# Performance work log

Measured on AMD Instinct MI355X. Metric: run time of the kernel, lower is better.

## Reference

```python
import jax, jax.numpy as jnp
import numpy as np


def setup_inputs() -> dict:
    key = jax.random.key(0)
    k1, k2 = jax.random.split(key)
    B, C, H, W = 16, 256, 64, 64
    K, D = 1024, 256
    z = jax.random.normal(k1, (B, C, H, W), dtype=jnp.float32)
    embedding = jax.random.normal(k2, (K, D), dtype=jnp.float32)
    return {"z": z, "embedding": embedding}


def reference(z, embedding):
    # _preprocess: shift channel dim (axis 1) to last, flatten -> [N, D]
    B, C, H, W = z.shape
    encoded_permuted = jnp.transpose(z, (0, 2, 3, 1))  # [B, H, W, C]
    permuted_shape = encoded_permuted.shape
    encoded_flat = encoded_permuted.reshape(-1, C)  # [N, D]

    x_sq = jnp.sum(encoded_flat * encoded_flat, axis=1, keepdims=True)  # [N, 1]
    e_sq = jnp.sum(embedding * embedding, axis=1)  # [K]
    cross = encoded_flat @ embedding.T  # [N, K]
    distances = x_sq - 2.0 * cross + e_sq[None, :]
    codebook_indices = jnp.argmin(distances, axis=1)  # [N]
    quantized_lookup = embedding[codebook_indices]  # [N, D]

    # straight-through estimator
    quantized_flat = encoded_flat + jax.lax.stop_gradient(quantized_lookup - encoded_flat)

    # _postprocess: reshape and shift last dim back to axis 1
    quantized = jnp.transpose(quantized_flat.reshape(permuted_shape), (0, 3, 1, 2))
    return (encoded_flat, quantized_flat, codebook_indices, quantized)
```

## Files before the change

kernel.cpp:

```cpp
#include <hip/hip_runtime.h>
#include <hip/hip_bf16.h>

typedef _Float16 h8 __attribute__((ext_vector_type(8)));
typedef float f4 __attribute__((ext_vector_type(4)));

#define N_TOK 65536
#define DIM 256
#define KCODES 1024
#define HWSZ 4096

__device__ __forceinline__ void gll16(const void* g, void* l) {
    __builtin_amdgcn_global_load_lds((const __attribute__((address_space(1))) void*)g,
                                     (__attribute__((address_space(3))) void*)l, 16, 0, 0);
}


__global__ void k_prep_frag(const float* __restrict__ emb, _Float16* __restrict__ BhF,
                            _Float16* __restrict__ BlF) {
    int gi = blockIdx.x * 256 + threadIdx.x;
    int kb = gi >> 9, s = (gi >> 6) & 7, dq = (gi >> 4) & 3, r = gi & 15;
    int code = kb * 16 + r;
    const float* src = emb + (size_t)code * DIM + s * 32 + dq * 8;
    float4 x0 = *(const float4*)(src);
    float4 x1 = *(const float4*)(src + 4);
    float xs[8] = {x0.x, x0.y, x0.z, x0.w, x1.x, x1.y, x1.z, x1.w};
    h8 hi, lo;
#pragma unroll
    for (int j = 0; j < 8; ++j) {
        _Float16 h = (_Float16)xs[j];
        hi[j] = h;
        lo[j] = (_Float16)(xs[j] - (float)h);
    }
    *(h8*)(BhF + (size_t)gi * 8) = hi;
    *(h8*)(BlF + (size_t)gi * 8) = lo;
}

__global__ void k_esq(const float* __restrict__ emb, float* __restrict__ e_sq) {
    int t = threadIdx.x;
    int code = blockIdx.x * 4 + (t >> 6);
    int l = t & 63;
    float4 v = *(const float4*)(emb + (size_t)code * DIM + l * 4);
    float s = v.x * v.x + v.y * v.y + v.z * v.z + v.w * v.w;
#pragma unroll
    for (int off = 32; off >= 1; off >>= 1) s += __shfl_xor(s, off);
    if (l == 0) e_sq[code] = s;
}

__global__ void k_transpose(const float* __restrict__ z, float* __restrict__ enc,
                            _Float16* __restrict__ AhF, _Float16* __restrict__ AlF) {
    __shared__ float T[64][65];
    int blk = blockIdx.x;
    int b = blk >> 8;
    int rem = blk & 255;
    int c0 = (rem >> 6) * 64;
    int hw0 = (rem & 63) * 64;
    int t = threadIdx.x;
    const float* zp = z + (size_t)b * DIM * HWSZ;
    {
        int hw4 = (t & 15) * 4, cl = t >> 4;
#pragma unroll
        for (int i = 0; i < 4; ++i) {
            int c = cl + i * 16;
            float4 v = *(const float4*)(zp + (size_t)(c0 + c) * HWSZ + hw0 + hw4);
            T[c][hw4 + 0] = v.x; T[c][hw4 + 1] = v.y;
            T[c][hw4 + 2] = v.z; T[c][hw4 + 3] = v.w;
        }
    }
    __syncthreads();
    {
        int c4 = (t & 15) * 4, hwl = t >> 4;
#pragma unroll
        for (int i = 0; i < 4; ++i) {
            int hw = hwl + i * 16;
            float4 v;
            v.x = T[c4 + 0][hw]; v.y = T[c4 + 1][hw];
            v.z = T[c4 + 2][hw]; v.w = T[c4 + 3][hw];
            *(float4*)(enc + (size_t)(b * HWSZ + hw0 + hw) * DIM + c0 + c4) = v;
        }
    }
    {
        int base_nb = b * 256 + (hw0 >> 4);
#pragma unroll
        for (int i = 0; i < 2; ++i) {
            int gidx = i * 256 + t;
            int nbi = gidx >> 7, si = (gidx >> 6) & 1, dq = (gidx >> 4) & 3, r = gidx & 15;
            int hwl = nbi * 16 + r;
            int cl = si * 32 + dq * 8;
            h8 hi, lo;
#pragma unroll
            for (int j = 0; j < 8; ++j) {
                float x = T[cl + j][hwl];
                _Float16 h = (_Float16)x;
                hi[j] = h;
                lo[j] = (_Float16)(x - (float)h);
            }
            size_t G = (((size_t)(base_nb + nbi) * 8) + (c0 >> 5) + si) * 64 + dq * 16 + r;
            *(h8*)(AhF + G * 8) = hi;
            *(h8*)(AlF + G * 8) = lo;
        }
    }
}

#define WAITV(n) asm volatile("s_waitcnt vmcnt(" #n ")" ::: "memory")
#define BARRIER __builtin_amdgcn_s_barrier()
#define PRIO1 __builtin_amdgcn_s_setprio(1)
#define PRIO0 __builtin_amdgcn_s_setprio(0)

extern __shared__ char SB[];

__global__ __launch_bounds__(1024)
void k_gemm_argmin(const _Float16* __restrict__ AhF, const _Float16* __restrict__ AlF,
                   const _Float16* __restrict__ BhF, const _Float16* __restrict__ BlF,
                   const float* __restrict__ e_sq,
                   float* __restrict__ pV1, int* __restrict__ pI1) {
    int gid = blockIdx.x;
    int grp = gid >> 7;
    int colTile = (gid >> 5) & 3;
    int rowTile = grp * 32 + (gid & 31);
    int r0 = rowTile * 256, c0 = colTile * 256;
    int t = threadIdx.x;
    int w = t >> 6, l = t & 63;
    int wm = w >> 2, wn = w & 3;
    int l16 = l & 15, lhi = l >> 4;

    const char* gAh = (const char*)AhF + (((size_t)(rowTile * 16 + w)) << 13) + (l << 4);
    const char* gAl = (const char*)AlF + (((size_t)(rowTile * 16 + w)) << 13) + (l << 4);
    const char* gBh = (const char*)BhF + (((size_t)(colTile * 16 + w)) << 13) + (l << 4);
    const char* gBl = (const char*)BlF + (((size_t)(colTile * 16 + w)) << 13) + (l << 4);

#define ISSUE_S(s) do { \
    char* bp_ = SB + ((s) & 1) * 65536; \
    gll16(gAh + ((s) << 10), bp_ + (w << 10)); \
    gll16(gBh + ((s) << 10), bp_ + 16384 + (w << 10)); \
    gll16(gAl + ((s) << 10), bp_ + 32768 + (w << 10)); \
    gll16(gBl + ((s) << 10), bp_ + 49152 + (w << 10)); \
} while (0)

#define MFMA16(A_, B_) { _Pragma("unroll") for (int mf = 0; mf < 4; ++mf) \
    _Pragma("unroll") for (int nf = 0; nf < 4; ++nf) \
        acc[mf][nf] = __builtin_amdgcn_mfma_f32_16x16x32_f16(A_[mf], B_[nf], acc[mf][nf], 0, 0, 0); }

#define PHASE(q, DO_ISSUE) { \
    WAITV(0); \
    BARRIER; \
    if (DO_ISSUE) ISSUE_S((q) + 1); \
    const char* bp_ = SB + ((q) & 1) * 65536; \
    _Pragma("unroll") for (int mf = 0; mf < 4; ++mf) \
        ah[mf] = *(const h8*)(bp_ + ((wm * 4 + mf) << 10) + (l << 4)); \
    _Pragma("unroll") for (int nf = 0; nf < 4; ++nf) \
        bh[nf] = *(const h8*)(bp_ + 16384 + ((wn * 4 + nf) << 10) + (l << 4)); \
    PRIO1; MFMA16(ah, bh); PRIO0; \
    { h8 xl[4]; \
      _Pragma("unroll") for (int nf = 0; nf < 4; ++nf) \
          xl[nf] = *(const h8*)(bp_ + 49152 + ((wn * 4 + nf) << 10) + (l << 4)); \
      PRIO1; MFMA16(ah, xl); PRIO0; \
      _Pragma("unroll") for (int mf = 0; mf < 4; ++mf) \
          xl[mf] = *(const h8*)(bp_ + 32768 + ((wm * 4 + mf) << 10) + (l << 4)); \
      PRIO1; MFMA16(xl, bh); PRIO0; } }

    f4 acc[4][4];
#pragma unroll
    for (int i = 0; i < 4; ++i)
#pragma unroll
        for (int j = 0; j < 4; ++j) acc[i][j] = (f4)0.0f;

    h8 ah[4], bh[4];

    ISSUE_S(0);

    PHASE(0, 1)  PHASE(1, 1)  PHASE(2, 1)  PHASE(3, 1)
    PHASE(4, 1)  PHASE(5, 1)  PHASE(6, 1)  PHASE(7, 0)

    float* smV = (float*)SB;
    int* smI = (int*)(SB + 4096);

    float esq[4];
#pragma unroll
    for (int nf = 0; nf < 4; ++nf) esq[nf] = e_sq[c0 + wn * 64 + nf * 16 + l16];

#pragma unroll
    for (int mf = 0; mf < 4; ++mf) {
#pragma unroll
        for (int rg = 0; rg < 4; ++rg) {
            float bestV = 3.4e38f;
            int bestI = 0;
#pragma unroll
            for (int nf = 0; nf < 4; ++nf) {
                float v = esq[nf] - 2.0f * acc[mf][nf][rg];
                int ci = c0 + wn * 64 + nf * 16 + l16;
                if (v < bestV || (v == bestV && ci < bestI)) { bestV = v; bestI = ci; }
            }
#pragma unroll
            for (int off = 1; off < 16; off <<= 1) {
                float vv = __shfl_xor(bestV, off);
                int ii = __shfl_xor(bestI, off);
                if (vv < bestV || (vv == bestV && ii < bestI)) { bestV = vv; bestI = ii; }
            }
            if (l16 == 0) {
                int rloc = wm * 64 + mf * 16 + lhi * 4 + rg;
                smV[wn * 256 + rloc] = bestV;
                smI[wn * 256 + rloc] = bestI;
            }
        }
    }
    __syncthreads();
    if (t < 256) {
        float bestV = smV[t];
        int bestI = smI[t];
#pragma unroll
        for (int wn2 = 1; wn2 < 4; ++wn2) {
            float v = smV[wn2 * 256 + t];
            int i2 = smI[wn2 * 256 + t];
            if (v < bestV || (v == bestV && i2 < bestI)) { bestV = v; bestI = i2; }
        }
        pV1[colTile * N_TOK + r0 + t] = bestV;
        pI1[colTile * N_TOK + r0 + t] = bestI;
    }
}

__global__ void k_final_all(const float* __restrict__ pV1, const int* __restrict__ pI1,
                            const float* __restrict__ emb,
                            float* __restrict__ out2, float* __restrict__ out1,
                            float* __restrict__ out3) {
    __shared__ int sidx[256];
    __shared__ float E[32][257];
    int t = threadIdx.x;
    int n0 = blockIdx.x * 256;
    int n = n0 + t;
    float v1 = pV1[n];
    int i1 = pI1[n];
#pragma unroll
    for (int ct = 1; ct < 4; ++ct) {
        float a1 = pV1[ct * N_TOK + n];
        int ai = pI1[ct * N_TOK + n];
        if (a1 < v1 || (a1 == v1 && ai < i1)) { v1 = a1; i1 = ai; }
    }
    out2[n] = (float)i1;
    sidx[t] = i1;
    __syncthreads();
    {
        int rr = t >> 2, q = t & 3;
#pragma unroll
        for (int i = 0; i < 4; ++i) {
            int r = i * 64 + rr;
            int idx = sidx[r];
            const float* src = emb + (size_t)idx * DIM + q * 64;
            float* dst = out1 + (size_t)(n0 + r) * DIM + q * 64;
#pragma unroll
            for (int j = 0; j < 16; ++j)
                *(float4*)(dst + j * 4) = *(const float4*)(src + j * 4);
        }
    }
    int b = n0 >> 12;
    int hw0b = n0 & 4095;
    for (int sub = 0; sub < 8; ++sub) {
        __syncthreads();
        {
            int r = t >> 3, oct = t & 7;
            int idx = sidx[sub * 32 + r];
            const float* src = emb + (size_t)idx * DIM + oct * 32;
#pragma unroll
            for (int i = 0; i < 8; ++i) {
                float4 v = *(const float4*)(src + i * 4);
                E[r][oct * 32 + i * 4 + 0] = v.x;
                E[r][oct * 32 + i * 4 + 1] = v.y;
                E[r][oct * 32 + i * 4 + 2] = v.z;
                E[r][oct * 32 + i * 4 + 3] = v.w;
            }
        }
        __syncthreads();
        {
            int w = t >> 6, l = t & 63;
            int ch = l >> 5, hw = l & 31;
            float* dst = out3 + (size_t)b * DIM * HWSZ + hw0b + sub * 32 + hw;
#pragma unroll
            for (int it = 0; it < 32; ++it) {
                int c = w * 64 + it * 2 + ch;
                dst[(size_t)c * HWSZ] = E[hw][c];
            }
        }
    }
}

extern "C" void kernel_launch(void* const* d_in, const int* in_sizes, int n_in,
                              void* d_out, int out_size, void* d_ws, size_t ws_size,
                              hipStream_t stream) {
    const float* z = (const float*)d_in[0];
    const float* emb = (const float*)d_in[1];
    float* out = (float*)d_out;
    float* out0 = out;
    float* out1 = out + 16777216;
    float* out2 = out + 33554432;
    float* out3 = out + 33619968;

    _Float16* AhF = (_Float16*)out1;
    _Float16* AlF = (_Float16*)(out1 + 8388608);

    char* ws = (char*)d_ws;
    _Float16* BhF = (_Float16*)(ws);
    _Float16* BlF = (_Float16*)(ws + 524288);
    float* e_sq = (float*)(ws + 1048576);
    float* pV1 = (float*)(ws + 1052672);
    int* pI1 = (int*)(ws + 2101248);

    hipFuncSetAttribute((const void*)k_gemm_argmin,
                        hipFuncAttributeMaxDynamicSharedMemorySize, 131072);

    k_prep_frag<<<128, 256, 0, stream>>>(emb, BhF, BlF);
    k_esq<<<256, 256, 0, stream>>>(emb, e_sq);
    k_transpose<<<4096, 256, 0, stream>>>(z, out0, AhF, AlF);
    k_gemm_argmin<<<1024, 1024, 131072, stream>>>(AhF, AlF, BhF, BlF, e_sq, pV1, pI1);
    k_final_all<<<256, 256, 0, stream>>>(pV1, pI1, emb, out2, out1, out3);
}
```

Measured before the change: 205.4 us.

## Shrink GEMM tiles to 128x128 and merge argmin partials via packed 64-bit atomicMin

The fused distance-GEMM/argmin kernel moves from 256x256 tiles with 1024 threads to 128x128 tiles with 512 threads and 64KB LDS, so more blocks can be resident per CU. Per-tile minima are packed into an order-preserving 64-bit key (float bits, then index) and merged with atomicMin into one array. The key array is initialised inside the e_sq kernel. This replaces the four-way partial arrays and simplifies the final gather kernel, which now handles 64 tokens per block. In exchange, the smaller tiles reload A and B more often per unit of compute, and the change adds atomic traffic.

```diff
diff --git a/kernel.cpp b/kernel.cpp
--- a/kernel.cpp
+++ b/kernel.cpp
@@ -35,8 +35,10 @@
     *(h8*)(BlF + (size_t)gi * 8) = lo;
 }
 
-__global__ void k_esq(const float* __restrict__ emb, float* __restrict__ e_sq) {
+__global__ void k_esq(const float* __restrict__ emb, float* __restrict__ e_sq,
+                      unsigned long long* __restrict__ key64) {
     int t = threadIdx.x;
+    key64[blockIdx.x * 256 + t] = ~0ull;
     int code = blockIdx.x * 4 + (t >> 6);
     int l = t & 63;
     float4 v = *(const float4*)(emb + (size_t)code * DIM + l * 4);
@@ -108,63 +110,64 @@
 
 extern __shared__ char SB[];
 
-__global__ __launch_bounds__(1024)
+__global__ __launch_bounds__(512, 4)
 void k_gemm_argmin(const _Float16* __restrict__ AhF, const _Float16* __restrict__ AlF,
                    const _Float16* __restrict__ BhF, const _Float16* __restrict__ BlF,
                    const float* __restrict__ e_sq,
-                   float* __restrict__ pV1, int* __restrict__ pI1) {
+                   unsigned long long* __restrict__ key64) {
     int gid = blockIdx.x;
-    int grp = gid >> 7;
-    int colTile = (gid >> 5) & 3;
-    int rowTile = grp * 32 + (gid & 31);
-    int r0 = rowTile * 256, c0 = colTile * 256;
+    int grp = gid >> 9;
+    int colTile = (gid >> 6) & 7;
+    int rowTile = grp * 64 + (gid & 63);
+    int r0 = rowTile * 128, c0 = colTile * 128;
     int t = threadIdx.x;
     int w = t >> 6, l = t & 63;
     int wm = w >> 2, wn = w & 3;
     int l16 = l & 15, lhi = l >> 4;
 
-    const char* gAh = (const char*)AhF + (((size_t)(rowTile * 16 + w)) << 13) + (l << 4);
-    const char* gAl = (const char*)AlF + (((size_t)(rowTile * 16 + w)) << 13) + (l << 4);
-    const char* gBh = (const char*)BhF + (((size_t)(colTile * 16 + w)) << 13) + (l << 4);
-    const char* gBl = (const char*)BlF + (((size_t)(colTile * 16 + w)) << 13) + (l << 4);
+    const char* gAh = (const char*)AhF + (((size_t)(rowTile * 8 + w)) << 13) + (l << 4);
+    const char* gAl = (const char*)AlF + (((size_t)(rowTile * 8 + w)) << 13) + (l << 4);
+    const char* gBh = (const char*)BhF + (((size_t)(colTile * 8 + w)) << 13) + (l << 4);
+    const char* gBl = (const char*)BlF + (((size_t)(colTile * 8 + w)) << 13) + (l << 4);
 
 #define ISSUE_S(s) do { \
-    char* bp_ = SB + ((s) & 1) * 65536; \
+    char* bp_ = SB + ((s) & 1) * 32768; \
     gll16(gAh + ((s) << 10), bp_ + (w << 10)); \
-    gll16(gBh + ((s) << 10), bp_ + 16384 + (w << 10)); \
-    gll16(gAl + ((s) << 10), bp_ + 32768 + (w << 10)); \
-    gll16(gBl + ((s) << 10), bp_ + 49152 + (w << 10)); \
+    gll16(gBh + ((s) << 10), bp_ + 8192 + (w << 10)); \
+    gll16(gAl + ((s) << 10), bp_ + 16384 + (w << 10)); \
+    gll16(gBl + ((s) << 10), bp_ + 24576 + (w << 10)); \
 } while (0)
 
-#define MFMA16(A_, B_) { _Pragma("unroll") for (int mf = 0; mf < 4; ++mf) \
-    _Pragma("unroll") for (int nf = 0; nf < 4; ++nf) \
+#define MFMA8(A_, B_) { _Pragma("unroll") for (int mf = 0; mf < 4; ++mf) \
+    _Pragma("unroll") for (int nf = 0; nf < 2; ++nf) \
         acc[mf][nf] = __builtin_amdgcn_mfma_f32_16x16x32_f16(A_[mf], B_[nf], acc[mf][nf], 0, 0, 0); }
 
 #define PHASE(q, DO_ISSUE) { \
     WAITV(0); \
     BARRIER; \
     if (DO_ISSUE) ISSUE_S((q) + 1); \
-    const char* bp_ = SB + ((q) & 1) * 65536; \
+    const char* bp_ = SB + ((q) & 1) * 32768; \
     _Pragma("unroll") for (int mf = 0; mf < 4; ++mf) \
         ah[mf] = *(const h8*)(bp_ + ((wm * 4 + mf) << 10) + (l << 4)); \
-    _Pragma("unroll") for (int nf = 0; nf < 4; ++nf) \
-        bh[nf] = *(const h8*)(bp_ + 16384 + ((wn * 4 + nf) << 10) + (l << 4)); \
-    PRIO1; MFMA16(ah, bh); PRIO0; \
-    { h8 xl[4]; \
-      _Pragma("unroll") for (int nf = 0; nf < 4; ++nf) \
-          xl[nf] = *(const h8*)(bp_ + 49152 + ((wn * 4 + nf) << 10) + (l << 4)); \
-      PRIO1; MFMA16(ah, xl); PRIO0; \
+    _Pragma("unroll") for (int nf = 0; nf < 2; ++nf) \
+        bh[nf] = *(const h8*)(bp_ + 8192 + ((wn * 2 + nf) << 10) + (l << 4)); \
+    PRIO1; MFMA8(ah, bh); PRIO0; \
+    { h8 xb[2]; \
+      _Pragma("unroll") for (int nf = 0; nf < 2; ++nf) \
+          xb[nf] = *(const h8*)(bp_ + 24576 + ((wn * 2 + nf) << 10) + (l << 4)); \
+      PRIO1; MFMA8(ah, xb); PRIO0; } \
+    { h8 xa[4]; \
       _Pragma("unroll") for (int mf = 0; mf < 4; ++mf) \
-          xl[mf] = *(const h8*)(bp_ + 32768 + ((wm * 4 + mf) << 10) + (l << 4)); \
-      PRIO1; MFMA16(xl, bh); PRIO0; } }
-
-    f4 acc[4][4];
+          xa[mf] = *(const h8*)(bp_ + 16384 + ((wm * 4 + mf) << 10) + (l << 4)); \
+      PRIO1; MFMA8(xa, bh); PRIO0; } }
+
+    f4 acc[4][2];
 #pragma unroll
     for (int i = 0; i < 4; ++i)
 #pragma unroll
-        for (int j = 0; j < 4; ++j) acc[i][j] = (f4)0.0f;
-
-    h8 ah[4], bh[4];
+        for (int j = 0; j < 2; ++j) acc[i][j] = (f4)0.0f;
+
+    h8 ah[4], bh[2];
 
     ISSUE_S(0);
 
@@ -172,11 +175,11 @@
     PHASE(4, 1)  PHASE(5, 1)  PHASE(6, 1)  PHASE(7, 0)
 
     float* smV = (float*)SB;
-    int* smI = (int*)(SB + 4096);
-
-    float esq[4];
-#pragma unroll
-    for (int nf = 0; nf < 4; ++nf) esq[nf] = e_sq[c0 + wn * 64 + nf * 16 + l16];
+    int* smI = (int*)(SB + 2048);
+
+    float esq[2];
+#pragma unroll
+    for (int nf = 0; nf < 2; ++nf) esq[nf] = e_sq[c0 + wn * 32 + nf * 16 + l16];
 
 #pragma unroll
     for (int mf = 0; mf < 4; ++mf) {
@@ -185,9 +188,9 @@
             float bestV = 3.4e38f;
             int bestI = 0;
 #pragma unroll
-            for (int nf = 0; nf < 4; ++nf) {
+            for (int nf = 0; nf < 2; ++nf) {
                 float v = esq[nf] - 2.0f * acc[mf][nf][rg];
-                int ci = c0 + wn * 64 + nf * 16 + l16;
+                int ci = c0 + wn * 32 + nf * 16 + l16;
                 if (v < bestV || (v == bestV && ci < bestI)) { bestV = v; bestI = ci; }
             }
 #pragma unroll
@@ -198,62 +201,54 @@
             }
             if (l16 == 0) {
                 int rloc = wm * 64 + mf * 16 + lhi * 4 + rg;
-                smV[wn * 256 + rloc] = bestV;
-                smI[wn * 256 + rloc] = bestI;
+                smV[wn * 128 + rloc] = bestV;
+                smI[wn * 128 + rloc] = bestI;
             }
         }
     }
     __syncthreads();
-    if (t < 256) {
+    if (t < 128) {
         float bestV = smV[t];
         int bestI = smI[t];
 #pragma unroll
         for (int wn2 = 1; wn2 < 4; ++wn2) {
-            float v = smV[wn2 * 256 + t];
-            int i2 = smI[wn2 * 256 + t];
+            float v = smV[wn2 * 128 + t];
+            int i2 = smI[wn2 * 128 + t];
             if (v < bestV || (v == bestV && i2 < bestI)) { bestV = v; bestI = i2; }
         }
-        pV1[colTile * N_TOK + r0 + t] = bestV;
-        pI1[colTile * N_TOK + r0 + t] = bestI;
-    }
-}
-
-__global__ void k_final_all(const float* __restrict__ pV1, const int* __restrict__ pI1,
+        unsigned int bu = __float_as_uint(bestV);
+        unsigned int u = (bu & 0x80000000u) ? ~bu : (bu | 0x80000000u);
+        unsigned long long key = ((unsigned long long)u << 10) | (unsigned int)bestI;
+        atomicMin(&key64[r0 + t], key);
+    }
+}
+
+__global__ void k_final_all(const unsigned long long* __restrict__ key64,
                             const float* __restrict__ emb,
                             float* __restrict__ out2, float* __restrict__ out1,
                             float* __restrict__ out3) {
-    __shared__ int sidx[256];
+    __shared__ int sidx[64];
     __shared__ float E[32][257];
     int t = threadIdx.x;
-    int n0 = blockIdx.x * 256;
-    int n = n0 + t;
-    float v1 = pV1[n];
-    int i1 = pI1[n];
-#pragma unroll
-    for (int ct = 1; ct < 4; ++ct) {
-        float a1 = pV1[ct * N_TOK + n];
-        int ai = pI1[ct * N_TOK + n];
-        if (a1 < v1 || (a1 == v1 && ai < i1)) { v1 = a1; i1 = ai; }
-    }
-    out2[n] = (float)i1;
-    sidx[t] = i1;
+    int n0 = blockIdx.x * 64;
+    if (t < 64) {
+        int idx = (int)(key64[n0 + t] & 1023ull);
+        out2[n0 + t] = (float)idx;
+        sidx[t] = idx;
+    }
     __syncthreads();
     {
-        int rr = t >> 2, q = t & 3;
-#pragma unroll
-        for (int i = 0; i < 4; ++i) {
-            int r = i * 64 + rr;
-            int idx = sidx[r];
-            const float* src = emb + (size_t)idx * DIM + q * 64;
-            float* dst = out1 + (size_t)(n0 + r) * DIM + q * 64;
-#pragma unroll
-            for (int j = 0; j < 16; ++j)
-                *(float4*)(dst + j * 4) = *(const float4*)(src + j * 4);
-        }
+        int r = t >> 2, q = t & 3;
+        int idx = sidx[r];
+        const float* src = emb + (size_t)idx * DIM + q * 64;
+        float* dst = out1 + (size_t)(n0 + r) * DIM + q * 64;
+#pragma unroll
+        for (int j = 0; j < 16; ++j)
+            *(float4*)(dst + j * 4) = *(const float4*)(src + j * 4);
     }
     int b = n0 >> 12;
     int hw0b = n0 & 4095;
-    for (int sub = 0; sub < 8; ++sub) {
+    for (int sub = 0; sub < 2; ++sub) {
         __syncthreads();
         {
             int r = t >> 3, oct = t & 7;
@@ -300,15 +295,14 @@
     _Float16* BhF = (_Float16*)(ws);
     _Float16* BlF = (_Float16*)(ws + 524288);
     float* e_sq = (float*)(ws + 1048576);
-    float* pV1 = (float*)(ws + 1052672);
-    int* pI1 = (int*)(ws + 2101248);
+    unsigned long long* key64 = (unsigned long long*)(ws + 1052672);
 
     hipFuncSetAttribute((const void*)k_gemm_argmin,
-                        hipFuncAttributeMaxDynamicSharedMemorySize, 131072);
+                        hipFuncAttributeMaxDynamicSharedMemorySize, 65536);
 
     k_prep_frag<<<128, 256, 0, stream>>>(emb, BhF, BlF);
-    k_esq<<<256, 256, 0, stream>>>(emb, e_sq);
+    k_esq<<<256, 256, 0, stream>>>(emb, e_sq, key64);
     k_transpose<<<4096, 256, 0, stream>>>(z, out0, AhF, AlF);
-    k_gemm_argmin<<<1024, 1024, 131072, stream>>>(AhF, AlF, BhF, BlF, e_sq, pV1, pI1);
-    k_final_all<<<256, 256, 0, stream>>>(pV1, pI1, emb, out2, out1, out3);
-}
+    k_gemm_argmin<<<4096, 512, 65536, stream>>>(AhF, AlF, BhF, BlF, e_sq, key64);
+    k_final_all<<<1024, 256, 0, stream>>>(key64, emb, out2, out1, out3);
+}
```

Result: slower. 253.2 us (+23.3%).

## Restructure GEMM-argmin into 8-wave blocks with 4-stage split-precision pipeline

Applied to the files above, without the earlier changes.

The fused distance GEMM now runs 512 threads per block instead of 1024, with each wave computing 128x64 outputs (8x4 MFMA tiles) instead of 64x64. The three split-fp16 products (hi*hi, hi*lo, lo*hi) are flattened into 24 K-chunks, each fed by a 4-deep LDS ring buffer. A and B prefetches are issued separately in the two halves of each chunk. The goal is more register-level reuse of B fragments and deeper overlap of global-to-LDS loads with MFMA work. The cost is doubled accumulator registers per wave and more barriers per chunk. The launch_bounds(512,2) hint cannot be met with 128KB of LDS per block.

```diff
diff --git a/kernel.cpp b/kernel.cpp
--- a/kernel.cpp
+++ b/kernel.cpp
@@ -105,10 +105,12 @@
 #define BARRIER __builtin_amdgcn_s_barrier()
 #define PRIO1 __builtin_amdgcn_s_setprio(1)
 #define PRIO0 __builtin_amdgcn_s_setprio(0)
+#define LGKM0 asm volatile("s_waitcnt lgkmcnt(0)" ::: "memory")
+#define SGB0 __builtin_amdgcn_sched_barrier(0)
 
 extern __shared__ char SB[];
 
-__global__ __launch_bounds__(1024)
+__global__ __launch_bounds__(512, 2)
 void k_gemm_argmin(const _Float16* __restrict__ AhF, const _Float16* __restrict__ AlF,
                    const _Float16* __restrict__ BhF, const _Float16* __restrict__ BlF,
                    const float* __restrict__ e_sq,
@@ -123,53 +125,59 @@
     int wm = w >> 2, wn = w & 3;
     int l16 = l & 15, lhi = l >> 4;
 
-    const char* gAh = (const char*)AhF + (((size_t)(rowTile * 16 + w)) << 13) + (l << 4);
-    const char* gAl = (const char*)AlF + (((size_t)(rowTile * 16 + w)) << 13) + (l << 4);
-    const char* gBh = (const char*)BhF + (((size_t)(colTile * 16 + w)) << 13) + (l << 4);
-    const char* gBl = (const char*)BlF + (((size_t)(colTile * 16 + w)) << 13) + (l << 4);
-
-#define ISSUE_S(s) do { \
-    char* bp_ = SB + ((s) & 1) * 65536; \
-    gll16(gAh + ((s) << 10), bp_ + (w << 10)); \
-    gll16(gBh + ((s) << 10), bp_ + 16384 + (w << 10)); \
-    gll16(gAl + ((s) << 10), bp_ + 32768 + (w << 10)); \
-    gll16(gBl + ((s) << 10), bp_ + 49152 + (w << 10)); \
-} while (0)
-
-#define MFMA16(A_, B_) { _Pragma("unroll") for (int mf = 0; mf < 4; ++mf) \
+    const char* gAh = (const char*)AhF + (((size_t)(rowTile * 16 + 2 * w)) << 13) + (l << 4);
+    const char* gAl = (const char*)AlF + (((size_t)(rowTile * 16 + 2 * w)) << 13) + (l << 4);
+    const char* gBh = (const char*)BhF + (((size_t)(colTile * 16 + 2 * w)) << 13) + (l << 4);
+    const char* gBl = (const char*)BlF + (((size_t)(colTile * 16 + 2 * w)) << 13) + (l << 4);
+
+#define ISSUE_A(c) do { const char* a_ = (((c) >> 3) == 2) ? gAl : gAh; \
+    char* bp_ = SB + ((c) & 3) * 32768 + ((2 * w) << 10); \
+    const int so_ = ((c) & 7) << 10; \
+    gll16(a_ + so_, bp_); gll16(a_ + 8192 + so_, bp_ + 1024); } while (0)
+
+#define ISSUE_B(c) do { const char* b_ = (((c) >> 3) == 1) ? gBl : gBh; \
+    char* bp_ = SB + ((c) & 3) * 32768 + 16384 + ((2 * w) << 10); \
+    const int so_ = ((c) & 7) << 10; \
+    gll16(b_ + so_, bp_); gll16(b_ + 8192 + so_, bp_ + 1024); } while (0)
+
+#define RD_A(c, mo) { const char* bp_ = SB + ((c) & 3) * 32768; \
+    _Pragma("unroll") for (int mf = 0; mf < 4; ++mf) \
+        ah[mf] = *(const h8*)(bp_ + ((wm * 8 + (mo) + mf) << 10) + (l << 4)); }
+
+#define RD_B(c) { const char* bp_ = SB + ((c) & 3) * 32768 + 16384; \
     _Pragma("unroll") for (int nf = 0; nf < 4; ++nf) \
-        acc[mf][nf] = __builtin_amdgcn_mfma_f32_16x16x32_f16(A_[mf], B_[nf], acc[mf][nf], 0, 0, 0); }
-
-#define PHASE(q, DO_ISSUE) { \
-    WAITV(0); \
+        bh[nf] = *(const h8*)(bp_ + ((wn * 4 + nf) << 10) + (l << 4)); }
+
+#define MFMA_HALF(mo) { _Pragma("unroll") for (int mf = 0; mf < 4; ++mf) \
+    _Pragma("unroll") for (int nf = 0; nf < 4; ++nf) \
+        acc[(mo) + mf][nf] = __builtin_amdgcn_mfma_f32_16x16x32_f16(ah[mf], bh[nf], acc[(mo) + mf][nf], 0, 0, 0); }
+
+#define CHUNK(c, W) \
+    WAITV(W); BARRIER; \
+    if ((c) <= 20) { ISSUE_A((c) + 3); } \
+    RD_A(c, 0); RD_B(c); \
+    LGKM0; SGB0; PRIO1; MFMA_HALF(0); PRIO0; \
     BARRIER; \
-    if (DO_ISSUE) ISSUE_S((q) + 1); \
-    const char* bp_ = SB + ((q) & 1) * 65536; \
-    _Pragma("unroll") for (int mf = 0; mf < 4; ++mf) \
-        ah[mf] = *(const h8*)(bp_ + ((wm * 4 + mf) << 10) + (l << 4)); \
-    _Pragma("unroll") for (int nf = 0; nf < 4; ++nf) \
-        bh[nf] = *(const h8*)(bp_ + 16384 + ((wn * 4 + nf) << 10) + (l << 4)); \
-    PRIO1; MFMA16(ah, bh); PRIO0; \
-    { h8 xl[4]; \
-      _Pragma("unroll") for (int nf = 0; nf < 4; ++nf) \
-          xl[nf] = *(const h8*)(bp_ + 49152 + ((wn * 4 + nf) << 10) + (l << 4)); \
-      PRIO1; MFMA16(ah, xl); PRIO0; \
-      _Pragma("unroll") for (int mf = 0; mf < 4; ++mf) \
-          xl[mf] = *(const h8*)(bp_ + 32768 + ((wm * 4 + mf) << 10) + (l << 4)); \
-      PRIO1; MFMA16(xl, bh); PRIO0; } }
-
-    f4 acc[4][4];
-#pragma unroll
-    for (int i = 0; i < 4; ++i)
+    if ((c) <= 20) { ISSUE_B((c) + 3); } \
+    RD_A(c, 4); \
+    LGKM0; SGB0; PRIO1; MFMA_HALF(4); PRIO0;
+
+    f4 acc[8][4];
+#pragma unroll
+    for (int i = 0; i < 8; ++i)
 #pragma unroll
         for (int j = 0; j < 4; ++j) acc[i][j] = (f4)0.0f;
 
     h8 ah[4], bh[4];
 
-    ISSUE_S(0);
-
-    PHASE(0, 1)  PHASE(1, 1)  PHASE(2, 1)  PHASE(3, 1)
-    PHASE(4, 1)  PHASE(5, 1)  PHASE(6, 1)  PHASE(7, 0)
+    ISSUE_A(0); ISSUE_B(0); ISSUE_A(1); ISSUE_B(1); ISSUE_A(2); ISSUE_B(2);
+
+    CHUNK(0, 8)   CHUNK(1, 8)   CHUNK(2, 8)   CHUNK(3, 8)
+    CHUNK(4, 8)   CHUNK(5, 8)   CHUNK(6, 8)   CHUNK(7, 8)
+    CHUNK(8, 8)   CHUNK(9, 8)   CHUNK(10, 8)  CHUNK(11, 8)
+    CHUNK(12, 8)  CHUNK(13, 8)  CHUNK(14, 8)  CHUNK(15, 8)
+    CHUNK(16, 8)  CHUNK(17, 8)  CHUNK(18, 8)  CHUNK(19, 8)
+    CHUNK(20, 8)  CHUNK(21, 8)  CHUNK(22, 4)  CHUNK(23, 0)
 
     float* smV = (float*)SB;
     int* smI = (int*)(SB + 4096);
@@ -179,7 +187,7 @@
     for (int nf = 0; nf < 4; ++nf) esq[nf] = e_sq[c0 + wn * 64 + nf * 16 + l16];
 
 #pragma unroll
-    for (int mf = 0; mf < 4; ++mf) {
+    for (int mf = 0; mf < 8; ++mf) {
 #pragma unroll
         for (int rg = 0; rg < 4; ++rg) {
             float bestV = 3.4e38f;
@@ -197,7 +205,7 @@
                 if (vv < bestV || (vv == bestV && ii < bestI)) { bestV = vv; bestI = ii; }
             }
             if (l16 == 0) {
-                int rloc = wm * 64 + mf * 16 + lhi * 4 + rg;
+                int rloc = wm * 128 + mf * 16 + lhi * 4 + rg;
                 smV[wn * 256 + rloc] = bestV;
                 smI[wn * 256 + rloc] = bestI;
             }
@@ -309,6 +317,6 @@
     k_prep_frag<<<128, 256, 0, stream>>>(emb, BhF, BlF);
     k_esq<<<256, 256, 0, stream>>>(emb, e_sq);
     k_transpose<<<4096, 256, 0, stream>>>(z, out0, AhF, AlF);
-    k_gemm_argmin<<<1024, 1024, 131072, stream>>>(AhF, AlF, BhF, BlF, e_sq, pV1, pI1);
+    k_gemm_argmin<<<1024, 512, 131072, stream>>>(AhF, AlF, BhF, BlF, e_sq, pV1, pI1);
     k_final_all<<<256, 256, 0, stream>>>(pV1, pI1, emb, out2, out1, out3);
 }
```

After: 222.3 us. 1.08x slower.

## Restructure GEMM-argmin to 8 waves with ping-pong staged split-fp16 pipeline

Applied to the files above, without the earlier changes.

Rewrites the fused distance GEMM main loop so each 512-thread block uses 8 waves, each owning a 128x64 output tile, in place of 16 waves owning 64x64. The K loop becomes 12 staged sub-tiles covering the hi*hi, hi*lo and lo*hi products, with separate A and B double buffers and asynchronous global-to-LDS loads issued between MFMA quadrants. Barriers and explicit lgkmcnt waits are placed so that loads overlap compute. The intent is more register reuse per LDS read and better overlap of memory and MFMA work. The cost is higher register pressure and more barriers, and a launch bound of two blocks per CU that the 128KB of LDS per block may not allow.

```diff
diff --git a/kernel.cpp b/kernel.cpp
--- a/kernel.cpp
+++ b/kernel.cpp
@@ -105,10 +105,12 @@
 #define BARRIER __builtin_amdgcn_s_barrier()
 #define PRIO1 __builtin_amdgcn_s_setprio(1)
 #define PRIO0 __builtin_amdgcn_s_setprio(0)
+#define LGKM0 do { asm volatile("s_waitcnt lgkmcnt(0)" ::: "memory"); \
+                   __builtin_amdgcn_sched_barrier(0); } while (0)
 
 extern __shared__ char SB[];
 
-__global__ __launch_bounds__(1024)
+__global__ __launch_bounds__(512, 2)
 void k_gemm_argmin(const _Float16* __restrict__ AhF, const _Float16* __restrict__ AlF,
                    const _Float16* __restrict__ BhF, const _Float16* __restrict__ BlF,
                    const float* __restrict__ e_sq,
@@ -128,78 +130,111 @@
     const char* gBh = (const char*)BhF + (((size_t)(colTile * 16 + w)) << 13) + (l << 4);
     const char* gBl = (const char*)BlF + (((size_t)(colTile * 16 + w)) << 13) + (l << 4);
 
-#define ISSUE_S(s) do { \
-    char* bp_ = SB + ((s) & 1) * 65536; \
-    gll16(gAh + ((s) << 10), bp_ + (w << 10)); \
-    gll16(gBh + ((s) << 10), bp_ + 16384 + (w << 10)); \
-    gll16(gAl + ((s) << 10), bp_ + 32768 + (w << 10)); \
-    gll16(gBl + ((s) << 10), bp_ + 49152 + (w << 10)); \
+#define ST_A(tau, h) do { \
+    const char* s_ = (((tau) >> 2) == 2) ? gAl : gAh; \
+    const int s0_ = ((tau) & 3) * 2; \
+    char* d_ = SB + (((tau) & 1) * 32768) + ((h) * 16384) + ((2 * w) << 10); \
+    gll16(s_ + ((h) << 16) + (s0_ << 10), d_); \
+    gll16(s_ + ((h) << 16) + ((s0_ + 1) << 10), d_ + 1024); \
 } while (0)
 
-#define MFMA16(A_, B_) { _Pragma("unroll") for (int mf = 0; mf < 4; ++mf) \
-    _Pragma("unroll") for (int nf = 0; nf < 4; ++nf) \
-        acc[mf][nf] = __builtin_amdgcn_mfma_f32_16x16x32_f16(A_[mf], B_[nf], acc[mf][nf], 0, 0, 0); }
-
-#define PHASE(q, DO_ISSUE) { \
-    WAITV(0); \
-    BARRIER; \
-    if (DO_ISSUE) ISSUE_S((q) + 1); \
-    const char* bp_ = SB + ((q) & 1) * 65536; \
-    _Pragma("unroll") for (int mf = 0; mf < 4; ++mf) \
-        ah[mf] = *(const h8*)(bp_ + ((wm * 4 + mf) << 10) + (l << 4)); \
-    _Pragma("unroll") for (int nf = 0; nf < 4; ++nf) \
-        bh[nf] = *(const h8*)(bp_ + 16384 + ((wn * 4 + nf) << 10) + (l << 4)); \
-    PRIO1; MFMA16(ah, bh); PRIO0; \
-    { h8 xl[4]; \
-      _Pragma("unroll") for (int nf = 0; nf < 4; ++nf) \
-          xl[nf] = *(const h8*)(bp_ + 49152 + ((wn * 4 + nf) << 10) + (l << 4)); \
-      PRIO1; MFMA16(ah, xl); PRIO0; \
-      _Pragma("unroll") for (int mf = 0; mf < 4; ++mf) \
-          xl[mf] = *(const h8*)(bp_ + 32768 + ((wm * 4 + mf) << 10) + (l << 4)); \
-      PRIO1; MFMA16(xl, bh); PRIO0; } }
-
-    f4 acc[4][4];
-#pragma unroll
-    for (int i = 0; i < 4; ++i)
-#pragma unroll
-        for (int j = 0; j < 4; ++j) acc[i][j] = (f4)0.0f;
-
-    h8 ah[4], bh[4];
-
-    ISSUE_S(0);
-
-    PHASE(0, 1)  PHASE(1, 1)  PHASE(2, 1)  PHASE(3, 1)
-    PHASE(4, 1)  PHASE(5, 1)  PHASE(6, 1)  PHASE(7, 0)
+#define ST_B(tau, h) do { \
+    const char* s_ = (((tau) >> 2) == 1) ? gBl : gBh; \
+    const int s0_ = ((tau) & 3) * 2; \
+    char* d_ = SB + 65536 + (((tau) & 1) * 32768) + ((h) * 16384) + ((2 * w) << 10); \
+    gll16(s_ + ((h) << 16) + (s0_ << 10), d_); \
+    gll16(s_ + ((h) << 16) + ((s0_ + 1) << 10), d_ + 1024); \
+} while (0)
+
+#define RD_A(tau, qm) { \
+    const char* p_ = SB + (((tau) & 1) * 32768) + (wm * 16384); \
+    _Pragma("unroll") for (int mf = 0; mf < 4; ++mf) { \
+        aR[mf * 2 + 0] = *(const h8*)(p_ + (((((qm) * 4 + mf) * 2) + 0) << 10) + (l << 4)); \
+        aR[mf * 2 + 1] = *(const h8*)(p_ + (((((qm) * 4 + mf) * 2) + 1) << 10) + (l << 4)); } }
+
+#define RD_B(tau, qn, bR) { \
+    const char* p_ = SB + 65536 + (((tau) & 1) * 32768) + ((wn >> 1) * 16384); \
+    _Pragma("unroll") for (int nf = 0; nf < 2; ++nf) { \
+        const int nb_ = ((wn & 1) * 4 + (qn) * 2 + nf) * 2; \
+        bR[nf * 2 + 0] = *(const h8*)(p_ + ((nb_ + 0) << 10) + (l << 4)); \
+        bR[nf * 2 + 1] = *(const h8*)(p_ + ((nb_ + 1) << 10) + (l << 4)); } }
+
+#define MM(qm, qn, bR) { _Pragma("unroll") for (int mf = 0; mf < 4; ++mf) \
+    _Pragma("unroll") for (int nf = 0; nf < 2; ++nf) { \
+        acc[qm][qn][mf][nf] = __builtin_amdgcn_mfma_f32_16x16x32_f16(aR[mf*2+0], bR[nf*2+0], acc[qm][qn][mf][nf], 0, 0, 0); \
+        acc[qm][qn][mf][nf] = __builtin_amdgcn_mfma_f32_16x16x32_f16(aR[mf*2+1], bR[nf*2+1], acc[qm][qn][mf][nf], 0, 0, 0); } }
+
+#define TILE(tau) { \
+    RD_A(tau, 0); RD_B(tau, 0, bQ0); \
+    if ((tau) + 1 < 12) { ST_A((tau) + 1, 1); } \
+    BARRIER; LGKM0; PRIO1; MM(0, 0, bQ0); PRIO0; BARRIER; \
+    RD_B(tau, 1, bQ1); \
+    BARRIER; LGKM0; PRIO1; MM(0, 1, bQ1); PRIO0; BARRIER; \
+    RD_A(tau, 1); \
+    if ((tau) + 2 < 12) { ST_B((tau) + 2, 0); } \
+    BARRIER; LGKM0; PRIO1; MM(1, 1, bQ1); PRIO0; BARRIER; \
+    if ((tau) + 2 < 12) { ST_B((tau) + 2, 1); ST_A((tau) + 2, 0); } \
+    PRIO1; MM(1, 0, bQ0); PRIO0; \
+    if ((tau) < 10) { WAITV(6); } else { WAITV(0); } \
+    BARRIER; }
+
+    f4 acc[2][2][4][2];
+#pragma unroll
+    for (int i = 0; i < 2; ++i)
+#pragma unroll
+        for (int j = 0; j < 2; ++j)
+#pragma unroll
+            for (int m = 0; m < 4; ++m)
+#pragma unroll
+                for (int n = 0; n < 2; ++n) acc[i][j][m][n] = (f4)0.0f;
+
+    h8 aR[8], bQ0[4], bQ1[4];
+
+    ST_B(0, 0); ST_B(0, 1); ST_A(0, 0); ST_A(0, 1);
+    ST_B(1, 0); ST_B(1, 1); ST_A(1, 0);
+    WAITV(6); BARRIER;
+
+    TILE(0)  TILE(1)  TILE(2)  TILE(3)
+    TILE(4)  TILE(5)  TILE(6)  TILE(7)
+    TILE(8)  TILE(9)  TILE(10) TILE(11)
 
     float* smV = (float*)SB;
     int* smI = (int*)(SB + 4096);
 
     float esq[4];
 #pragma unroll
-    for (int nf = 0; nf < 4; ++nf) esq[nf] = e_sq[c0 + wn * 64 + nf * 16 + l16];
-
-#pragma unroll
-    for (int mf = 0; mf < 4; ++mf) {
-#pragma unroll
-        for (int rg = 0; rg < 4; ++rg) {
-            float bestV = 3.4e38f;
-            int bestI = 0;
-#pragma unroll
-            for (int nf = 0; nf < 4; ++nf) {
-                float v = esq[nf] - 2.0f * acc[mf][nf][rg];
-                int ci = c0 + wn * 64 + nf * 16 + l16;
-                if (v < bestV || (v == bestV && ci < bestI)) { bestV = v; bestI = ci; }
-            }
-#pragma unroll
-            for (int off = 1; off < 16; off <<= 1) {
-                float vv = __shfl_xor(bestV, off);
-                int ii = __shfl_xor(bestI, off);
-                if (vv < bestV || (vv == bestV && ii < bestI)) { bestV = vv; bestI = ii; }
-            }
-            if (l16 == 0) {
-                int rloc = wm * 64 + mf * 16 + lhi * 4 + rg;
-                smV[wn * 256 + rloc] = bestV;
-                smI[wn * 256 + rloc] = bestI;
+    for (int qn = 0; qn < 2; ++qn)
+#pragma unroll
+        for (int nf = 0; nf < 2; ++nf)
+            esq[qn * 2 + nf] = e_sq[c0 + wn * 64 + qn * 32 + nf * 16 + l16];
+
+#pragma unroll
+    for (int qm = 0; qm < 2; ++qm) {
+#pragma unroll
+        for (int mf = 0; mf < 4; ++mf) {
+#pragma unroll
+            for (int rg = 0; rg < 4; ++rg) {
+                float bestV = 3.4e38f;
+                int bestI = 0;
+#pragma unroll
+                for (int qn = 0; qn < 2; ++qn)
+#pragma unroll
+                    for (int nf = 0; nf < 2; ++nf) {
+                        float v = esq[qn * 2 + nf] - 2.0f * acc[qm][qn][mf][nf][rg];
+                        int ci = c0 + wn * 64 + qn * 32 + nf * 16 + l16;
+                        if (v < bestV || (v == bestV && ci < bestI)) { bestV = v; bestI = ci; }
+                    }
+#pragma unroll
+                for (int off = 1; off < 16; off <<= 1) {
+                    float vv = __shfl_xor(bestV, off);
+                    int ii = __shfl_xor(bestI, off);
+                    if (vv < bestV || (vv == bestV && ii < bestI)) { bestV = vv; bestI = ii; }
+                }
+                if (l16 == 0) {
+                    int rloc = wm * 128 + qm * 64 + mf * 16 + lhi * 4 + rg;
+                    smV[wn * 256 + rloc] = bestV;
+                    smI[wn * 256 + rloc] = bestI;
+                }
             }
         }
     }
@@ -309,6 +344,6 @@
     k_prep_frag<<<128, 256, 0, stream>>>(emb, BhF, BlF);
     k_esq<<<256, 256, 0, stream>>>(emb, e_sq);
     k_transpose<<<4096, 256, 0, stream>>>(z, out0, AhF, AlF);
-    k_gemm_argmin<<<1024, 1024, 131072, stream>>>(AhF, AlF, BhF, BlF, e_sq, pV1, pI1);
+    k_gemm_argmin<<<1024, 512, 131072, stream>>>(AhF, AlF, BhF, BlF, e_sq, pV1, pI1);
     k_final_all<<<256, 256, 0, stream>>>(pV1, pI1, emb, out2, out1, out3);
 }
```

After: 240.4 us. 1.17x slower.
